# Performance work log

Measured on AMD Instinct MI355X. Metric: run time of the kernel, lower is better.

## Reference

```python
import jax, jax.numpy as jnp
import numpy as np
from jax import lax

DN = ('NCHW', 'OIHW', 'NCHW')

def conv(x, w, stride=1):
    return lax.conv_general_dilated(x, w, (stride, stride), 'SAME', dimension_numbers=DN)

def setup_inputs() -> dict:
    key = jax.random.key(0)
    ks = jax.random.split(key, 8)
    B, Cin, H, W = 16, 3, 512, 512
    Cenc, Cdec, n_heads, n_classes = 64, 64, 5, 1
    s = lambda *shape: 0.05
    return {
        'x': jax.random.normal(ks[0], (B, Cin, H, W), jnp.float32),
        'cls_id': jax.random.randint(ks[1], (B,), 0, n_heads, jnp.int32),
        'enc_w': jax.random.normal(ks[2], (Cenc, Cin, 3, 3), jnp.float32) * 0.1,
        'enc_b': jax.random.normal(ks[3], (Cenc,), jnp.float32) * 0.1,
        'dec_w': jax.random.normal(ks[4], (Cdec, Cenc, 3, 3), jnp.float32) * 0.05,
        'dec_b': jax.random.normal(ks[5], (Cdec,), jnp.float32) * 0.1,
        'head_w': jax.random.normal(ks[6], (n_heads, n_classes, Cdec, 3, 3), jnp.float32) * 0.05,
        'head_b': jax.random.normal(ks[7], (n_heads, n_classes), jnp.float32) * 0.1,
    }

def reference(x, cls_id, enc_w, enc_b, dec_w, dec_b, head_w, head_b):
    # encoder: stride-2 conv + relu -> features  [B, Cenc, H/2, W/2]
    f = jax.nn.relu(conv(x, enc_w, 2) + enc_b[None, :, None, None])
    # decoder: 3x3 conv + relu -> decoder_output [B, Cdec, H/2, W/2]
    d = jax.nn.relu(conv(f, dec_w, 1) + dec_b[None, :, None, None])
    # routing: apply segmentation_head[cls_id[b]] to sample b.
    # (gather-by-id -> per-head conv -> backsort) == per-sample gathered-kernel conv
    wk = head_w[cls_id]  # [B, n_classes, Cdec, 3, 3]
    bk = head_b[cls_id]  # [B, n_classes]
    def one_sample(di, wi):  # di: [Cdec,Hd,Wd], wi: [n_classes,Cdec,3,3]
        return conv(di[None], wi, 1)[0]
    masks = jax.vmap(one_sample)(d, wk) + bk[:, :, None, None]
    return masks  # [B, n_classes, H/2, W/2]
```

## Files before the change

kernel.cpp:

```cpp
#include <hip/hip_runtime.h>
#include <stdint.h>

#define NIMG 16
#define HIN 512
#define WIN 512
#define HO 256
#define WO 256
#define HP 258
#define WP 258

typedef unsigned short bf16_t;
typedef unsigned int u32;
typedef short bf16x8 __attribute__((ext_vector_type(8)));
typedef float f32x4 __attribute__((ext_vector_type(4)));
typedef float f32x16 __attribute__((ext_vector_type(16)));


static __device__ __forceinline__ bf16_t f2bf(float f) {
    u32 u = __float_as_uint(f);
    u += 0x7FFFu + ((u >> 16) & 1u);
    return (bf16_t)(u >> 16);
}
static __device__ __forceinline__ float bf_lo(u32 u) { return __uint_as_float(u << 16); }
static __device__ __forceinline__ float bf_hi(u32 u) { return __uint_as_float(u & 0xFFFF0000u); }
static __device__ __forceinline__ u32 pack2(float a, float b) {
    return (u32)f2bf(a) | ((u32)f2bf(b) << 16);
}

__global__ void repack_w(const float* __restrict__ dec_w, const float* __restrict__ enc_w,
                         bf16_t* __restrict__ wB, bf16_t* __restrict__ wEB) {
    int i = blockIdx.x * 256 + threadIdx.x;
    if (i < 36864) {
        int j  = i & 7;
        int l  = (i >> 3) & 63;
        int q  = (i >> 9) & 1;
        int kc = (i >> 10) & 3;
        int r  = i >> 12;
        int co  = q * 32 + (l & 31);
        int pos = kc * 16 + ((l >> 5) & 1) * 8 + j;
        int ci  = (pos & 1) * 32 + (pos >> 1);
        wB[i] = f2bf(dec_w[(co * 64 + ci) * 9 + r]);
    } else if (i < 36864 + 2048) {
        int t = i - 36864;
        int j = t & 7;
        int l = (t >> 3) & 63;
        int n = (t >> 9) & 1;
        int s = (t >> 10) & 1;
        int co = n * 32 + (l & 31);
        int k  = s * 16 + ((l >> 5) & 1) * 8 + j;
        wEB[t] = (k < 27) ? f2bf(enc_w[co * 27 + k]) : (bf16_t)0;
    }
}

__global__ void zero_halo(bf16_t* __restrict__ buf, int nimg) {
    const int per_img = 1028 * 8;
    int i = blockIdx.x * 256 + threadIdx.x;
    if (i >= nimg * per_img) return;
    int z = i / per_img;
    int rem = i - z * per_img;
    int p = rem >> 3, q = rem & 7;
    int row, col;
    if (p < 258)      { row = 0;           col = p; }
    else if (p < 516) { row = 257;         col = p - 258; }
    else if (p < 772) { row = p - 516 + 1; col = 0; }
    else              { row = p - 772 + 1; col = 257; }
    *(uint4*)(buf + ((size_t)z * HP * WP + (size_t)row * WP + col) * 64 + q * 8) =
        make_uint4(0u, 0u, 0u, 0u);
}

__global__ __launch_bounds__(512) void encoder_mfma(
    const float* __restrict__ x, const bf16_t* __restrict__ wEB,
    const float* __restrict__ enc_b, bf16_t* __restrict__ f, int b0)
{
    __shared__ __align__(16) bf16_t xt[3][33][34];

    const int tid = threadIdx.x;
    const int w   = tid >> 6;
    const int l   = tid & 63;
    const int z   = blockIdx.z;
    const int b   = b0 + z;
    const int Y0  = blockIdx.y << 5;
    const int X0  = blockIdx.x << 5;

    const int col = l & 31;
    const float bias0 = enc_b[col];
    const float bias1 = enc_b[32 + col];

    const bf16x8* wv = (const bf16x8*)wEB;
    bf16x8 Bf[2][2];
    #pragma unroll
    for (int s = 0; s < 2; ++s) {
        Bf[s][0] = wv[((s * 2 + 0) << 6) + l];
        Bf[s][1] = wv[((s * 2 + 1) << 6) + l];
    }

    const float* xb = x + (size_t)b * 3 * HIN * WIN;
    for (int i = tid; i < 3267; i += 512) {
        int ci  = i / 1089;
        int rem = i - ci * 1089;
        int yy  = rem / 33, xx = rem - yy * 33;
        int iy = Y0 + yy, ix = X0 + xx;
        float v = (iy < HIN && ix < WIN)
                ? xb[(size_t)ci * HIN * WIN + (size_t)iy * WIN + ix] : 0.f;
        xt[ci][yy][xx] = f2bf(v);
    }
    __syncthreads();

    const int row = l & 31;
    const int py  = 2 * w + (row >> 4);
    const int px  = row & 15;
    const int kh  = (l >> 5) * 8;
    bf16x8 A[2];
    #pragma unroll
    for (int s = 0; s < 2; ++s) {
        #pragma unroll
        for (int j = 0; j < 8; ++j) {
            int k = s * 16 + kh + j;
            k = k < 27 ? k : 26;
            int ci  = (k * 29) >> 8;
            int tap = k - ci * 9;
            int dy  = (tap * 11) >> 5;
            int dx  = tap - dy * 3;
            A[s][j] = (short)xt[ci][2 * py + dy][2 * px + dx];
        }
    }

    f32x16 acc[2];
    acc[0] = (f32x16){0.f,0.f,0.f,0.f,0.f,0.f,0.f,0.f,0.f,0.f,0.f,0.f,0.f,0.f,0.f,0.f};
    acc[1] = acc[0];
    acc[0] = __builtin_amdgcn_mfma_f32_32x32x16_bf16(A[0], Bf[0][0], acc[0], 0, 0, 0);
    acc[1] = __builtin_amdgcn_mfma_f32_32x32x16_bf16(A[0], Bf[0][1], acc[1], 0, 0, 0);
    acc[0] = __builtin_amdgcn_mfma_f32_32x32x16_bf16(A[1], Bf[1][0], acc[0], 0, 0, 0);
    acc[1] = __builtin_amdgcn_mfma_f32_32x32x16_bf16(A[1], Bf[1][1], acc[1], 0, 0, 0);

    bf16_t* fz = f + (size_t)z * HP * WP * 64;
    const int by = blockIdx.y << 4, bx = blockIdx.x << 4;
    #pragma unroll
    for (int v = 0; v < 16; ++v) {
        const int grow = (v & 3) + 8 * (v >> 2) + 4 * (l >> 5);
        const int flat = w * 32 + grow;
        const int pyy = flat >> 4, pxx = flat & 15;
        float t0 = acc[0][v] + bias0;  t0 = t0 > 0.f ? t0 : 0.f;
        float t1 = acc[1][v] + bias1;  t1 = t1 > 0.f ? t1 : 0.f;
        *(u32*)(fz + ((size_t)(by + pyy + 1) * WP + (bx + pxx + 1)) * 64 + 2 * col) =
            pack2(t0, t1);
    }
}

__global__ __launch_bounds__(512, 6) void decoder_mfma(
    const bf16_t* __restrict__ f, const bf16_t* __restrict__ wB,
    const float* __restrict__ dec_b, bf16_t* __restrict__ d)
{
    __shared__ __align__(16) bf16_t tile[18 * 18 * 64];

    const int tid = threadIdx.x;
    const int w   = tid >> 6;
    const int l   = tid & 63;
    const int z   = blockIdx.z;
    const int y0  = blockIdx.y << 4, x0 = blockIdx.x << 4;

    const int col = l & 31;
    const float bias0 = dec_b[col];
    const float bias1 = dec_b[32 + col];

    const bf16_t* fbase = f + ((size_t)z * HP * WP + (size_t)y0 * WP + x0) * 64;
    for (int i = tid; i < 2592; i += 512) {
        int p   = i >> 3, qq = i & 7;
        int yy  = p / 18, xx = p - yy * 18;
        uint4 v = *(const uint4*)(fbase + ((size_t)yy * WP + xx) * 64 + qq * 8);
        int byteoff = (p * 128 + qq * 16) ^ ((p & 7) << 4);
        *(uint4*)((char*)tile + byteoff) = v;
    }

    f32x16 acc[2];
    acc[0] = (f32x16){0.f,0.f,0.f,0.f,0.f,0.f,0.f,0.f,0.f,0.f,0.f,0.f,0.f,0.f,0.f,0.f};
    acc[1] = acc[0];

    __syncthreads();

    const bf16x8* wBv = (const bf16x8*)wB;
    const int ty_l = (l >> 4) & 1;
    const int tx_l = l & 15;
    const int kh16 = (l >> 5) << 4;

    #pragma unroll
    for (int r = 0; r < 9; ++r) {
        const int dy = r / 3, dx = r - 3 * (r / 3);
        bf16x8 Bf[4][2];
        #pragma unroll
        for (int kc = 0; kc < 4; ++kc) {
            Bf[kc][0] = wBv[(((r * 4 + kc) << 1) + 0) * 64 + l];
            Bf[kc][1] = wBv[(((r * 4 + kc) << 1) + 1) * 64 + l];
        }
        const int p   = (2 * w + ty_l + dy) * 18 + tx_l + dx;
        const int swz = (p & 7) << 4;
        const int pb  = p * 128 + kh16;
        #pragma unroll
        for (int kc = 0; kc < 4; ++kc) {
            bf16x8 a = *(const bf16x8*)((const char*)tile + ((pb + kc * 32) ^ swz));
            acc[0] = __builtin_amdgcn_mfma_f32_32x32x16_bf16(a, Bf[kc][0], acc[0], 0, 0, 0);
            acc[1] = __builtin_amdgcn_mfma_f32_32x32x16_bf16(a, Bf[kc][1], acc[1], 0, 0, 0);
        }
    }

    bf16_t* dz = d + (size_t)z * HP * WP * 64;
    #pragma unroll
    for (int v = 0; v < 16; ++v) {
        const int grow = (v & 3) + 8 * (v >> 2) + 4 * (l >> 5);
        const int flat = w * 32 + grow;
        const int py = flat >> 4, px = flat & 15;
        float t0 = acc[0][v] + bias0;  t0 = t0 > 0.f ? t0 : 0.f;
        float t1 = acc[1][v] + bias1;  t1 = t1 > 0.f ? t1 : 0.f;
        *(u32*)(dz + ((size_t)(y0 + py + 1) * WP + (x0 + px + 1)) * 64 + 2 * col) =
            pack2(t0, t1);
    }
}

__global__ __launch_bounds__(256) void head_kernel(
    const bf16_t* __restrict__ d, const float* __restrict__ head_w,
    const float* __restrict__ head_b, const int* __restrict__ cls_id,
    float* __restrict__ out, int b0)
{
    __shared__ __align__(16) bf16_t tile[18 * 18 * 64];
    __shared__ float hw[9][64];

    const int tid = threadIdx.x;
    const int z   = blockIdx.z;
    const int b   = b0 + z;
    const int y0  = blockIdx.y << 4, x0 = blockIdx.x << 4;
    const int cls = cls_id[b];

    for (int i = tid; i < 576; i += 256) {
        int r = i >> 6, s = i & 63;
        int ci = (s & 1) * 32 + (s >> 1);
        hw[r][s] = head_w[((size_t)cls * 64 + ci) * 9 + r];
    }
    const bf16_t* dbase = d + ((size_t)z * HP * WP + (size_t)y0 * WP + x0) * 64;
    for (int i = tid; i < 2592; i += 256) {
        int yy  = i / 144;
        int rem = i - yy * 144;
        int xx  = rem >> 3, q = rem & 7;
        int p   = yy * 18 + xx;
        uint4 v = *(const uint4*)(dbase + ((size_t)yy * WP + xx) * 64 + q * 8);
        int byteoff = (p * 128 + q * 16) ^ ((p & 7) << 4);
        *(uint4*)((char*)tile + byteoff) = v;
    }
    __syncthreads();

    const int py = tid >> 4, px = tid & 15;
    float a0 = 0.f, a1 = 0.f, a2 = 0.f, a3 = 0.f;
    #pragma unroll 1
    for (int r = 0; r < 9; ++r) {
        const int dy = r / 3, dx = r - 3 * (r / 3);
        const int p  = (py + dy) * 18 + px + dx;
        const int swz = (p & 7) << 4;
        const float* wr = &hw[r][0];
        #pragma unroll
        for (int q = 0; q < 8; ++q) {
            uint4 v = *(const uint4*)((const char*)tile + ((p * 128 + q * 16) ^ swz));
            float4 w0 = *(const float4*)(wr + q * 8);
            float4 w1 = *(const float4*)(wr + q * 8 + 4);
            float t0 = fmaf(bf_lo(v.x), w0.x, fmaf(bf_hi(v.x), w0.y, 0.f));
            float t1 = fmaf(bf_lo(v.y), w0.z, fmaf(bf_hi(v.y), w0.w, 0.f));
            float t2 = fmaf(bf_lo(v.z), w1.x, fmaf(bf_hi(v.z), w1.y, 0.f));
            float t3 = fmaf(bf_lo(v.w), w1.z, fmaf(bf_hi(v.w), w1.w, 0.f));
            a0 += t0; a1 += t1; a2 += t2; a3 += t3;
        }
    }
    const float acc = head_b[cls] + (a0 + a1) + (a2 + a3);
    out[(size_t)b * (HO * WO) + (size_t)(y0 + py) * WO + (x0 + px)] = acc;
}

extern "C" void kernel_launch(void* const* d_in, const int* in_sizes, int n_in,
                              void* d_out, int out_size, void* d_ws, size_t ws_size,
                              hipStream_t stream) {
    const float* x      = (const float*)d_in[0];
    const int*   cls_id = (const int*)  d_in[1];
    const float* enc_w  = (const float*)d_in[2];
    const float* enc_b  = (const float*)d_in[3];
    const float* dec_w  = (const float*)d_in[4];
    const float* dec_b  = (const float*)d_in[5];
    const float* head_w = (const float*)d_in[6];
    const float* head_b = (const float*)d_in[7];
    float* out = (float*)d_out;

    const size_t WB_RESERVE = 131072;
    const size_t PER_IMG    = (size_t)HP * WP * 64 * 2;
    char* ws = (char*)d_ws;
    bf16_t* wB  = (bf16_t*)ws;
    bf16_t* wEB = (bf16_t*)(ws + 81920);

    size_t avail = (ws_size > WB_RESERVE) ? (ws_size - WB_RESERVE) : 0;
    int C = (int)(avail / (2 * PER_IMG));
    if (C < 1) C = 1;
    if (C > NIMG) C = NIMG;

    bf16_t* fbuf = (bf16_t*)(ws + WB_RESERVE);
    bf16_t* dbuf = (bf16_t*)(ws + WB_RESERVE + (size_t)C * PER_IMG);

    repack_w<<<dim3(152), 256, 0, stream>>>(dec_w, enc_w, wB, wEB);
    {
        int nthr = C * 1028 * 8;
        int nblk = (nthr + 255) / 256;
        zero_halo<<<dim3(nblk), 256, 0, stream>>>(fbuf, C);
        zero_halo<<<dim3(nblk), 256, 0, stream>>>(dbuf, C);
    }

    int n_rounds = (NIMG + C - 1) / C;
    int per = (NIMG + n_rounds - 1) / n_rounds;
    for (int b0 = 0; b0 < NIMG; b0 += per) {
        const int n = (NIMG - b0 < per) ? (NIMG - b0) : per;
        encoder_mfma<<<dim3(16, 16, n), 512, 0, stream>>>(x, wEB, enc_b, fbuf, b0);
        decoder_mfma<<<dim3(16, 16, n), 512, 0, stream>>>(fbuf, wB, dec_b, dbuf);
        head_kernel <<<dim3(16, 16, n), 256, 0, stream>>>(dbuf, head_w, head_b, cls_id, out, b0);
    }
}
```

Measured before the change: 234.6 us.

## Halve decoder and head tile heights and split head channels across lane pairs

The decoder and head kernels now work on 8x16 output tiles instead of 16x16, so they launch twice as many blocks, with 256 threads each and smaller LDS tiles. The head kernel gives each output pixel to two threads, each summing half of the channel chunks, and combines them with a lane shuffle. It also folds the FMAs into running accumulators. The aim is higher occupancy and more parallelism per CU, at the cost of more halo re-reads (10 rows loaded per 8 output rows instead of 18 per 16).

```diff
diff --git a/kernel.cpp b/kernel.cpp
--- a/kernel.cpp
+++ b/kernel.cpp
@@ -147,24 +147,25 @@
     }
 }
 
-__global__ __launch_bounds__(512, 6) void decoder_mfma(
+__global__ __launch_bounds__(256, 6) void decoder_mfma(
     const bf16_t* __restrict__ f, const bf16_t* __restrict__ wB,
     const float* __restrict__ dec_b, bf16_t* __restrict__ d)
 {
-    __shared__ __align__(16) bf16_t tile[18 * 18 * 64];
+    __shared__ __align__(16) bf16_t tile[10 * 18 * 64];
 
     const int tid = threadIdx.x;
     const int w   = tid >> 6;
     const int l   = tid & 63;
     const int z   = blockIdx.z;
-    const int y0  = blockIdx.y << 4, x0 = blockIdx.x << 4;
+    const int y0  = blockIdx.y << 3;
+    const int x0  = blockIdx.x << 4;
 
     const int col = l & 31;
     const float bias0 = dec_b[col];
     const float bias1 = dec_b[32 + col];
 
     const bf16_t* fbase = f + ((size_t)z * HP * WP + (size_t)y0 * WP + x0) * 64;
-    for (int i = tid; i < 2592; i += 512) {
+    for (int i = tid; i < 1440; i += 256) {
         int p   = i >> 3, qq = i & 7;
         int yy  = p / 18, xx = p - yy * 18;
         uint4 v = *(const uint4*)(fbase + ((size_t)yy * WP + xx) * 64 + qq * 8);
@@ -216,18 +217,19 @@
     }
 }
 
-__global__ __launch_bounds__(256) void head_kernel(
+__global__ __launch_bounds__(256, 6) void head_kernel(
     const bf16_t* __restrict__ d, const float* __restrict__ head_w,
     const float* __restrict__ head_b, const int* __restrict__ cls_id,
     float* __restrict__ out, int b0)
 {
-    __shared__ __align__(16) bf16_t tile[18 * 18 * 64];
+    __shared__ __align__(16) bf16_t tile[10 * 18 * 64];
     __shared__ float hw[9][64];
 
     const int tid = threadIdx.x;
     const int z   = blockIdx.z;
     const int b   = b0 + z;
-    const int y0  = blockIdx.y << 4, x0 = blockIdx.x << 4;
+    const int y0  = blockIdx.y << 3;
+    const int x0  = blockIdx.x << 4;
     const int cls = cls_id[b];
 
     for (int i = tid; i < 576; i += 256) {
@@ -236,39 +238,43 @@
         hw[r][s] = head_w[((size_t)cls * 64 + ci) * 9 + r];
     }
     const bf16_t* dbase = d + ((size_t)z * HP * WP + (size_t)y0 * WP + x0) * 64;
-    for (int i = tid; i < 2592; i += 256) {
-        int yy  = i / 144;
-        int rem = i - yy * 144;
-        int xx  = rem >> 3, q = rem & 7;
-        int p   = yy * 18 + xx;
+    for (int i = tid; i < 1440; i += 256) {
+        int p   = i >> 3, q = i & 7;
+        int yy  = p / 18, xx = p - yy * 18;
         uint4 v = *(const uint4*)(dbase + ((size_t)yy * WP + xx) * 64 + q * 8);
         int byteoff = (p * 128 + q * 16) ^ ((p & 7) << 4);
         *(uint4*)((char*)tile + byteoff) = v;
     }
     __syncthreads();
 
-    const int py = tid >> 4, px = tid & 15;
+    const int half = tid & 1;
+    const int px   = tid >> 1;
+    const int py   = px >> 4, pxx = px & 15;
     float a0 = 0.f, a1 = 0.f, a2 = 0.f, a3 = 0.f;
     #pragma unroll 1
     for (int r = 0; r < 9; ++r) {
         const int dy = r / 3, dx = r - 3 * (r / 3);
-        const int p  = (py + dy) * 18 + px + dx;
+        const int p  = (py + dy) * 18 + pxx + dx;
         const int swz = (p & 7) << 4;
         const float* wr = &hw[r][0];
         #pragma unroll
-        for (int q = 0; q < 8; ++q) {
+        for (int qi = 0; qi < 4; ++qi) {
+            const int q = 4 * half + qi;
             uint4 v = *(const uint4*)((const char*)tile + ((p * 128 + q * 16) ^ swz));
             float4 w0 = *(const float4*)(wr + q * 8);
             float4 w1 = *(const float4*)(wr + q * 8 + 4);
-            float t0 = fmaf(bf_lo(v.x), w0.x, fmaf(bf_hi(v.x), w0.y, 0.f));
-            float t1 = fmaf(bf_lo(v.y), w0.z, fmaf(bf_hi(v.y), w0.w, 0.f));
-            float t2 = fmaf(bf_lo(v.z), w1.x, fmaf(bf_hi(v.z), w1.y, 0.f));
-            float t3 = fmaf(bf_lo(v.w), w1.z, fmaf(bf_hi(v.w), w1.w, 0.f));
-            a0 += t0; a1 += t1; a2 += t2; a3 += t3;
+            a0 = fmaf(bf_lo(v.x), w0.x, fmaf(bf_hi(v.x), w0.y, a0));
+            a1 = fmaf(bf_lo(v.y), w0.z, fmaf(bf_hi(v.y), w0.w, a1));
+            a2 = fmaf(bf_lo(v.z), w1.x, fmaf(bf_hi(v.z), w1.y, a2));
+            a3 = fmaf(bf_lo(v.w), w1.z, fmaf(bf_hi(v.w), w1.w, a3));
         }
     }
-    const float acc = head_b[cls] + (a0 + a1) + (a2 + a3);
-    out[(size_t)b * (HO * WO) + (size_t)(y0 + py) * WO + (x0 + px)] = acc;
+    float tot = (a0 + a1) + (a2 + a3);
+    tot += __shfl_xor(tot, 1);
+    if (half == 0) {
+        out[(size_t)b * (HO * WO) + (size_t)(y0 + py) * WO + (x0 + pxx)] =
+            head_b[cls] + tot;
+    }
 }
 
 extern "C" void kernel_launch(void* const* d_in, const int* in_sizes, int n_in,
@@ -311,7 +317,7 @@
     for (int b0 = 0; b0 < NIMG; b0 += per) {
         const int n = (NIMG - b0 < per) ? (NIMG - b0) : per;
         encoder_mfma<<<dim3(16, 16, n), 512, 0, stream>>>(x, wEB, enc_b, fbuf, b0);
-        decoder_mfma<<<dim3(16, 16, n), 512, 0, stream>>>(fbuf, wB, dec_b, dbuf);
-        head_kernel <<<dim3(16, 16, n), 256, 0, stream>>>(dbuf, head_w, head_b, cls_id, out, b0);
-    }
-}
+        decoder_mfma<<<dim3(16, 32, n), 256, 0, stream>>>(fbuf, wB, dec_b, dbuf);
+        head_kernel <<<dim3(16, 32, n), 256, 0, stream>>>(dbuf, head_w, head_b, cls_id, out, b0);
+    }
+}
```

New measurement: 231.9 us. About the same (-1.1%).
